# Kernel optimization log

Measured on AMD Instinct MI355X. Metric: run time of the kernel, lower is better.

Reference implementation:

```python
import jax, jax.numpy as jnp
import numpy as np

N = 50000   # nodes
E = 400000  # edges
D = 256     # embedding_dimension
R = 2       # num_relations
NE = 2      # num experts
OUT = 256   # output_size
NEG_SLOPE = 0.01  # nn.LeakyReLU default


def setup_inputs() -> dict:
    key = jax.random.key(0)
    ks = jax.random.split(key, 18)
    s = 0.05
    inp = {
        "des": jax.random.normal(ks[0], (N, 128), jnp.float32),
        "tweet": jax.random.normal(ks[1], (N, 64), jnp.float32),
        "num_prop": jax.random.normal(ks[2], (N, 32), jnp.float32),
        "cat_prop": jax.random.normal(ks[3], (N, 32), jnp.float32),
        "edge_index": jax.random.randint(ks[4], (2, E), 0, N, jnp.int64),
        "edge_type": jax.random.randint(ks[5], (E,), 0, R, jnp.int64),
        # linear_relu_input
        "W_in": jax.random.normal(ks[6], (D, D), jnp.float32) * s,
        "b_in": jnp.zeros((D,), jnp.float32),
        # RGCNConv (shared across the two calls)
        "W_rel": jax.random.normal(ks[7], (R, D, D), jnp.float32) * s,
        "W_root": jax.random.normal(ks[8], (D, D), jnp.float32) * s,
        "b_rgcn": jnp.zeros((D,), jnp.float32),
        # MoE gate + experts (MLP: D -> D -> OUT)
        "w_gate": jax.random.normal(ks[9], (D, NE), jnp.float32) * s,
        "We1": jax.random.normal(ks[10], (NE, D, D), jnp.float32) * s,
        "be1": jnp.zeros((NE, D), jnp.float32),
        "We2": jax.random.normal(ks[11], (NE, D, OUT), jnp.float32) * s,
        "be2": jnp.zeros((NE, OUT), jnp.float32),
    }
    return inp


def _rgcn(x, W_rel, W_root, b, src, dst, edge_type):
    # per-relation node transform, then gather per edge; mean-aggregate per (node, relation)
    h = jnp.einsum('nd,rdh->rnh', x, W_rel)          # (R, N, D)
    msg = h[edge_type, src]                           # (E, D)
    seg = dst * R + edge_type                         # combined (node, relation) segment id
    sums = jax.ops.segment_sum(msg, seg, num_segments=N * R)
    cnt = jax.ops.segment_sum(jnp.ones((E,), msg.dtype), seg, num_segments=N * R)
    agg = sums / jnp.maximum(cnt, 1.0)[:, None]       # per-relation mean (0 if no edges)
    agg = agg.reshape(N, R, -1).sum(axis=1)           # sum over relations
    return x @ W_root + b + agg


def _moe(x, w_gate, We1, be1, We2, be2, k=1):
    # clean (eval) top-k gating: softmax over the top-k logits, scattered into zeros
    logits = x @ w_gate                               # (N, NE)
    top_vals, top_idx = jax.lax.top_k(logits, k)
    gate_vals = jax.nn.softmax(top_vals, axis=-1)     # k=1 -> weight 1.0
    gates = jnp.zeros_like(logits).at[jnp.arange(x.shape[0])[:, None], top_idx].set(gate_vals)
    # compute all experts densely (zero gates annihilate unselected experts)
    h1 = jnp.einsum('nd,edh->enh', x, We1) + be1[:, None, :]
    h1 = jnp.where(h1 >= 0, h1, NEG_SLOPE * h1)       # LeakyReLU
    ye = jnp.einsum('enh,eho->eno', h1, We2) + be2[:, None, :]
    return jnp.einsum('ne,eno->no', gates, ye)


def reference(des, tweet, num_prop, cat_prop, edge_index, edge_type,
              W_in, b_in, W_rel, W_root, b_rgcn, w_gate, We1, be1, We2, be2):
    src, dst = edge_index[0], edge_index[1]
    x = jnp.concatenate((des, tweet, num_prop, cat_prop), axis=1)  # (N, D)
    x = jax.nn.selu(x @ W_in + b_in)
    x = _rgcn(x, W_rel, W_root, b_rgcn, src, dst, edge_type)
    # dropout is identity in eval mode
    x = _rgcn(x, W_rel, W_root, b_rgcn, src, dst, edge_type)
    y = _moe(x, w_gate, We1, be1, We2, be2, k=1)
    return y
```

## Files before the change

kernel.cpp:

```cpp
#include <hip/hip_runtime.h>
#include <cstddef>

static constexpr int N_NODES = 50000;
static constexpr int N_EDGES = 400000;
static constexpr int D = 256;
static constexpr int R = 2;
static constexpr int M_PAD = 50048;
static constexpr int CAP = 32;
static constexpr int NSEG = N_NODES * R;

typedef _Float16 f16x8 __attribute__((ext_vector_type(8)));
typedef short bf16x8 __attribute__((ext_vector_type(8)));
typedef float f32x4 __attribute__((ext_vector_type(4)));

__device__ __forceinline__ unsigned short f2h(float f) {
    _Float16 h = (_Float16)f;
    return *(unsigned short*)&h;
}
__device__ __forceinline__ float h2f(unsigned short u) {
    _Float16 h = *(_Float16*)&u;
    return (float)h;
}
__device__ __forceinline__ unsigned short f2bf(float f) {
    unsigned u = __float_as_uint(f);
    u += 0x7FFF + ((u >> 16) & 1);
    return (unsigned short)(u >> 16);
}
__device__ __forceinline__ float bf2f(unsigned short h) {
    return __uint_as_float((unsigned)h << 16);
}

#define GLOAD16(g, l)                                                          \
    __builtin_amdgcn_global_load_lds(                                          \
        (const __attribute__((address_space(1))) void*)(g),                    \
        (__attribute__((address_space(3))) void*)(l), 16, 0, 0)

struct SSlab { const float* x; int xstr; int kstart; int mload; };
struct SArgs {
    SSlab sl[4];
    int nslab;
    const unsigned short* wt;
    int Ktot;
    int M;
    const float* bias;
    void* out;
};

template<int ACT>
__global__ __launch_bounds__(256, 2)
void sgemm(SArgs a) {
    __shared__ unsigned short As[3][128 * 32];
    __shared__ unsigned short Bs[3][128 * 32];
    const int tid  = threadIdx.x;
    const int wave = tid >> 6, lane = tid & 63;
    const int wm = wave >> 1, wn = wave & 1;
    const int row0 = blockIdx.x * 128;
    const int n0   = blockIdx.y * 128;

    const int arow  = tid >> 1;
    const int ahalf = tid & 1;
    const int br_   = tid >> 2;
    const int bg_   = tid & 3;

    const int gk   = lane >> 4;
    const int frow = lane & 15;
    const int fslot = (gk ^ ((frow >> 1) & 3)) << 3;

    f32x4 acc[4][4] = {};

    for (int ks = 0; ks < a.Ktot; ks += 32) {
        int s = a.nslab - 1;
        while (s > 0 && ks < a.sl[s].kstart) --s;
        const float* xb = a.sl[s].x;
        const int xstr  = a.sl[s].xstr;
        const int kloc  = ks - a.sl[s].kstart;
        const int mload = a.sl[s].mload;

        float ev[16];
        {
            const int gr = row0 + arow;
            if (gr < mload) {
                const float* ap = xb + (size_t)gr * xstr + kloc + ahalf * 16;
                *(float4*)&ev[0]  = ((const float4*)ap)[0];
                *(float4*)&ev[4]  = ((const float4*)ap)[1];
                *(float4*)&ev[8]  = ((const float4*)ap)[2];
                *(float4*)&ev[12] = ((const float4*)ap)[3];
            } else {
                #pragma unroll
                for (int j = 0; j < 16; ++j) ev[j] = 0.f;
            }
        }

        __syncthreads();

        #pragma unroll
        for (int p = 0; p < 3; ++p) {
            #pragma unroll
            for (int q = 0; q < 2; ++q) {
                const int r = q * 64 + br_;
                const int gsrc = (bg_ ^ ((r >> 1) & 3)) << 3;
                GLOAD16(a.wt + (size_t)p * 256 * a.Ktot + (size_t)(n0 + r) * a.Ktot + ks + gsrc,
                        &Bs[p][(q * 64 + wave * 16) * 32]);
            }
        }

        {
            const int sswz = (arow >> 1) & 3;
            #pragma unroll
            for (int g = 0; g < 2; ++g) {
                union { bf16x8 v; unsigned short u[8]; } p1, p2, p3;
                #pragma unroll
                for (int j = 0; j < 8; ++j) {
                    const float v = ev[g * 8 + j];
                    const unsigned short h1 = f2bf(v);
                    const float r1 = v - bf2f(h1);
                    const unsigned short h2 = f2bf(r1);
                    const float r2 = r1 - bf2f(h2);
                    p1.u[j] = h1; p2.u[j] = h2; p3.u[j] = f2bf(r2);
                }
                const int slot = ((ahalf * 2 + g) ^ sswz) << 3;
                *(bf16x8*)&As[0][arow * 32 + slot] = p1.v;
                *(bf16x8*)&As[1][arow * 32 + slot] = p2.v;
                *(bf16x8*)&As[2][arow * 32 + slot] = p3.v;
            }
        }

        __syncthreads();

        bf16x8 bq[4][3];
        #pragma unroll
        for (int n = 0; n < 4; ++n) {
            const int rr = wn * 64 + n * 16 + frow;
            #pragma unroll
            for (int p = 0; p < 3; ++p)
                bq[n][p] = *(const bf16x8*)&Bs[p][rr * 32 + fslot];
        }
        #pragma unroll
        for (int m = 0; m < 4; ++m) {
            const int rr = wm * 64 + m * 16 + frow;
            const bf16x8 a1 = *(const bf16x8*)&As[0][rr * 32 + fslot];
            const bf16x8 a2 = *(const bf16x8*)&As[1][rr * 32 + fslot];
            const bf16x8 a3 = *(const bf16x8*)&As[2][rr * 32 + fslot];
            #pragma unroll
            for (int n = 0; n < 4; ++n) {
                acc[m][n] = __builtin_amdgcn_mfma_f32_16x16x32_bf16(a1, bq[n][0], acc[m][n], 0, 0, 0);
                acc[m][n] = __builtin_amdgcn_mfma_f32_16x16x32_bf16(a1, bq[n][1], acc[m][n], 0, 0, 0);
                acc[m][n] = __builtin_amdgcn_mfma_f32_16x16x32_bf16(a2, bq[n][0], acc[m][n], 0, 0, 0);
                acc[m][n] = __builtin_amdgcn_mfma_f32_16x16x32_bf16(a1, bq[n][2], acc[m][n], 0, 0, 0);
                acc[m][n] = __builtin_amdgcn_mfma_f32_16x16x32_bf16(a3, bq[n][0], acc[m][n], 0, 0, 0);
                acc[m][n] = __builtin_amdgcn_mfma_f32_16x16x32_bf16(a2, bq[n][1], acc[m][n], 0, 0, 0);
            }
        }
    }

    const int erow = (lane >> 4) * 4;
    const int ecol = lane & 15;
    #pragma unroll
    for (int m = 0; m < 4; ++m) {
        #pragma unroll
        for (int r = 0; r < 4; ++r) {
            const int grow = row0 + wm * 64 + m * 16 + erow + r;
            if (grow >= a.M) continue;
            #pragma unroll
            for (int n = 0; n < 4; ++n) {
                const int gcol = n0 + wn * 64 + n * 16 + ecol;
                float v = acc[m][n][r] + a.bias[gcol];
                if (ACT == 1) {
                    const float scale = 1.0507009873554804934f;
                    const float alpha = 1.6732632423543772848f;
                    v = (v > 0.f) ? scale * v : scale * alpha * (expf(v) - 1.f);
                }
                ((float*)a.out)[(size_t)grow * 256 + gcol] = v;
            }
        }
    }
}

struct HSlab { const void* x; int xstr; int kstart; };
struct HArgs {
    HSlab sl[3];
    int nslab;
    const unsigned short* wt;
    int Ktot, M;
    const float* bias;
    const int* sel;
    void* out;
    int ldc;
};

template<int ACT, bool MASK, bool SELB, bool OUTF16, bool A32, bool EZ>
__global__ __launch_bounds__(256, 2)
void hgemm(HArgs a) {
    __shared__ unsigned short As[128 * 64];
    __shared__ unsigned short Bs[128 * 64];
    const int tid  = threadIdx.x;
    const int wave = tid >> 6, lane = tid & 63;
    const int wm = wave >> 1, wn = wave & 1;
    const int row0 = blockIdx.x * 128;
    const int n0   = blockIdx.y * 128;
    const int ex   = EZ ? (int)blockIdx.z : 0;
    const unsigned short* wt = a.wt + (size_t)ex * 65536;
    const float* bias = a.bias + ex * 256;

    const int srow = lane >> 3;
    const int scol = ((lane & 7) ^ (lane >> 3)) << 3;
    const int arow  = tid >> 1;
    const int ahalf = tid & 1;

    f32x4 acc[4][4] = {};

    for (int k0 = 0; k0 < a.Ktot; k0 += 64) {
        int s = a.nslab - 1;
        while (s > 0 && k0 < a.sl[s].kstart) --s;
        const int kloc = k0 - a.sl[s].kstart;
        const int xstr = a.sl[s].xstr;

        float ev[32];
        if (A32) {
            const float* xp = (const float*)a.sl[s].x;
            const float* ap = xp + (size_t)(row0 + arow) * xstr + kloc + ahalf * 32;
            #pragma unroll
            for (int q = 0; q < 8; ++q)
                *(float4*)&ev[q * 4] = ((const float4*)ap)[q];
        }

        __syncthreads();

        if (!A32) {
            const unsigned short* xp = (const unsigned short*)a.sl[s].x;
            #pragma unroll
            for (int i = 0; i < 4; ++i) {
                const int r = wave * 32 + i * 8;
                GLOAD16(xp + (size_t)(row0 + r + srow) * xstr + kloc + scol, &As[r * 64]);
            }
        }
        #pragma unroll
        for (int i = 0; i < 4; ++i) {
            const int r = wave * 32 + i * 8;
            GLOAD16(wt + (size_t)(n0 + r + srow) * a.Ktot + k0 + scol, &Bs[r * 64]);
        }
        if (A32) {
            #pragma unroll
            for (int gi = 0; gi < 4; ++gi) {
                const int sgr = ahalf * 4 + gi;
                union { f16x8 v; _Float16 h[8]; } pk;
                #pragma unroll
                for (int j = 0; j < 8; ++j) pk.h[j] = (_Float16)ev[gi * 8 + j];
                *(f16x8*)&As[arow * 64 + ((sgr ^ (arow & 7)) << 3)] = pk.v;
            }
        }

        __syncthreads();

        #pragma unroll
        for (int kk = 0; kk < 2; ++kk) {
            const int gkk = kk * 4 + (lane >> 4);
            f16x8 af[4], bfr[4];
            #pragma unroll
            for (int m = 0; m < 4; ++m) {
                const int rr = wm * 64 + m * 16 + (lane & 15);
                af[m] = *(const f16x8*)&As[rr * 64 + ((gkk ^ (rr & 7)) << 3)];
            }
            #pragma unroll
            for (int n = 0; n < 4; ++n) {
                const int rr = wn * 64 + n * 16 + (lane & 15);
                bfr[n] = *(const f16x8*)&Bs[rr * 64 + ((gkk ^ (rr & 7)) << 3)];
            }
            #pragma unroll
            for (int m = 0; m < 4; ++m)
                #pragma unroll
                for (int n = 0; n < 4; ++n)
                    acc[m][n] = __builtin_amdgcn_mfma_f32_16x16x32_f16(
                        af[m], bfr[n], acc[m][n], 0, 0, 0);
        }
    }

    const int erow = (lane >> 4) * 4;
    const int ecol = lane & 15;
    #pragma unroll
    for (int m = 0; m < 4; ++m) {
        #pragma unroll
        for (int r = 0; r < 4; ++r) {
            const int grow = row0 + wm * 64 + m * 16 + erow + r;
            if (grow >= a.M) continue;
            int sv = 0;
            if (MASK || SELB) sv = a.sel[grow];
            #pragma unroll
            for (int n = 0; n < 4; ++n) {
                const int gcol = n0 + wn * 64 + n * 16 + ecol;
                const float b = SELB ? a.bias[sv * 256 + gcol] : bias[gcol];
                float v = acc[m][n][r] + b;
                if (ACT == 2) v = (v >= 0.f) ? v : 0.01f * v;
                if (MASK && sv != ex) v = 0.f;
                const size_t oidx = (size_t)grow * a.ldc + (EZ ? ex * 256 : 0) + gcol;
                if (OUTF16) ((unsigned short*)a.out)[oidx] = f2h(v);
                else        ((float*)a.out)[oidx] = v;
            }
        }
    }
}

__global__ __launch_bounds__(256)
void csr_build(const int* __restrict__ ei, const int* __restrict__ et,
               int* cnt, int* slots) {
    const int e = blockIdx.x * 256 + threadIdx.x;
    if (e >= N_EDGES) return;
    const int src = ei[e];
    const int dst = ei[N_EDGES + e];
    const int seg = dst * R + et[e];
    const int slot = atomicAdd(&cnt[seg], 1);
    if (slot < CAP) slots[(size_t)seg * CAP + slot] = src;
}

__global__ __launch_bounds__(256)
void aggregate(const float* __restrict__ X, const int* __restrict__ cnt,
               const int* __restrict__ slots, float* __restrict__ Ab,
               int seg0, int nseg) {
    const int w = blockIdx.x * 4 + (threadIdx.x >> 6);
    if (w >= nseg) return;
    const int lane = threadIdx.x & 63;
    const int s = seg0 + w;
    const int m = min(cnt[s], CAP);
    const int* sl = slots + (size_t)s * CAP;
    float4 acc = make_float4(0.f, 0.f, 0.f, 0.f);
    for (int i = 0; i < m; ++i) {
        const float4 v = *(const float4*)(X + (size_t)sl[i] * 256 + lane * 4);
        acc.x += v.x; acc.y += v.y; acc.z += v.z; acc.w += v.w;
    }
    const float inv = (m > 0) ? 1.0f / (float)m : 0.0f;
    acc.x *= inv; acc.y *= inv; acc.z *= inv; acc.w *= inv;
    *(float4*)(Ab + (size_t)(w >> 1) * 512 + (w & 1) * 256 + lane * 4) = acc;
}

__global__ __launch_bounds__(256)
void agg_h(const unsigned short* __restrict__ Xh, const int* __restrict__ cnt,
           const int* __restrict__ slots, unsigned short* __restrict__ Abh) {
    const int w = blockIdx.x * 4 + (threadIdx.x >> 6);
    if (w >= NSEG) return;
    const int lane = threadIdx.x & 63;
    const int m = min(cnt[w], CAP);
    const int* sl = slots + (size_t)w * CAP;
    float ac[4] = {};
    for (int i = 0; i < m; ++i) {
        const ushort4 v = *(const ushort4*)(Xh + (size_t)sl[i] * 256 + lane * 4);
        ac[0] += h2f(v.x); ac[1] += h2f(v.y); ac[2] += h2f(v.z); ac[3] += h2f(v.w);
    }
    const float inv = (m > 0) ? 1.0f / (float)m : 0.0f;
    ushort4 o = make_ushort4(f2h(ac[0] * inv), f2h(ac[1] * inv),
                             f2h(ac[2] * inv), f2h(ac[3] * inv));
    *(ushort4*)(Abh + (size_t)(w >> 1) * 512 + (w & 1) * 256 + lane * 4) = o;
}

__global__ __launch_bounds__(256)
void fold1(const float* __restrict__ W_root, const float* __restrict__ W_rel,
           const float* __restrict__ b_rg, const float* __restrict__ wg,
           float* __restrict__ wfold, float* __restrict__ c3) {
    const int idx = blockIdx.x * 256 + threadIdx.x;
    if (idx < 1536) {
        const int d = idx / 6, jj = idx % 6, c = jj >> 1, j = jj & 1;
        const float* row = (c == 0) ? W_root + (size_t)d * 256
                                    : W_rel + (size_t)(c - 1) * 65536 + (size_t)d * 256;
        float s = 0.f;
        for (int e = 0; e < 256; ++e) s += row[e] * wg[e * 2 + j];
        wfold[idx] = s;
    } else if (idx < 1538) {
        const int j = idx - 1536;
        float s = 0.f;
        for (int e = 0; e < 256; ++e) s += b_rg[e] * wg[e * 2 + j];
        c3[j] = s;
    }
}

__global__ __launch_bounds__(256)
void fold2(const float* __restrict__ W_root, const float* __restrict__ W_rel,
           const float* __restrict__ b_rg, const float* __restrict__ wfold,
           float* __restrict__ W6, float* __restrict__ cb) {
    const int idx = blockIdx.x * 256 + threadIdx.x;
    if (idx < 4608) {
        const int k = idx / 6, j = idx % 6;
        const float* row = (k < 256) ? W_root + (size_t)k * 256
                                     : W_rel + (size_t)(k - 256) * 256;
        float s = 0.f;
        for (int d = 0; d < 256; ++d) s += row[d] * wfold[d * 6 + j];
        W6[idx] = s;
    } else if (idx < 4614) {
        const int j = idx - 4608;
        float s = 0.f;
        for (int d = 0; d < 256; ++d) s += b_rg[d] * wfold[d * 6 + j];
        cb[j] = s;
    }
}

__global__ __launch_bounds__(256)
void vu_kernel(const float* __restrict__ X1, const float* __restrict__ Ab,
               const float* __restrict__ W6, float* __restrict__ VU, int M) {
    __shared__ float wl[768 * 6];
    for (int i = threadIdx.x; i < 768 * 6; i += 256) wl[i] = W6[i];
    __syncthreads();
    const int wave = threadIdx.x >> 6, lane = threadIdx.x & 63;
    const int n = blockIdx.x * 4 + wave;
    if (n >= M) return;
    const float4 xv = ((const float4*)(X1 + (size_t)n * 256))[lane];
    const float4 a0 = ((const float4*)(Ab + (size_t)n * 512))[lane];
    const float4 a1 = ((const float4*)(Ab + (size_t)n * 512))[lane + 64];
    const float xa[12] = {xv.x, xv.y, xv.z, xv.w, a0.x, a0.y, a0.z, a0.w,
                          a1.x, a1.y, a1.z, a1.w};
    float z[6] = {};
    #pragma unroll
    for (int t = 0; t < 3; ++t)
        #pragma unroll
        for (int i = 0; i < 4; ++i) {
            const int k = t * 256 + lane * 4 + i;
            #pragma unroll
            for (int j = 0; j < 6; ++j) z[j] = fmaf(xa[t * 4 + i], wl[k * 6 + j], z[j]);
        }
    #pragma unroll
    for (int off = 32; off; off >>= 1)
        #pragma unroll
        for (int j = 0; j < 6; ++j) z[j] += __shfl_down(z[j], off, 64);
    if (lane == 0) {
        #pragma unroll
        for (int j = 0; j < 6; ++j) VU[(size_t)n * 6 + j] = z[j];
    }
}

__global__ __launch_bounds__(256)
void u_gate(const float* __restrict__ VU, const int* __restrict__ cnt,
            const int* __restrict__ slots, const float* __restrict__ cb,
            const float* __restrict__ c3, int* __restrict__ sel, int M) {
    const int n = blockIdx.x * 256 + threadIdx.x;
    if (n >= M) return;
    float z0 = VU[(size_t)n * 6 + 0] + cb[0] + c3[0];
    float z1 = VU[(size_t)n * 6 + 1] + cb[1] + c3[1];
    #pragma unroll
    for (int r = 0; r < 2; ++r) {
        const int seg = n * 2 + r;
        const int m = min(cnt[seg], CAP);
        if (m > 0) {
            const int* sl = slots + (size_t)seg * CAP;
            float s0 = 0.f, s1 = 0.f;
            for (int i = 0; i < m; ++i) {
                const int src = sl[i];
                s0 += VU[(size_t)src * 6 + 2 + 2 * r];
                s1 += VU[(size_t)src * 6 + 3 + 2 * r];
            }
            const float inv = 1.0f / (float)m;
            z0 += s0 * inv + cb[2 + 2 * r];
            z1 += s1 * inv + cb[3 + 2 * r];
        }
    }
    sel[n] = (z1 > z0) ? 1 : 0;
}

struct WJ3 { const float* src[4]; unsigned short* dst[4]; int ktot[4]; int koff[4]; };
__global__ __launch_bounds__(256)
void wconv3(WJ3 j) {
    const int job = blockIdx.y;
    const int i = blockIdx.x * 256 + threadIdx.x;
    const int k = i >> 8, n = i & 255;
    const float v = j.src[job][i];
    const unsigned short h1 = f2bf(v);
    const float r1 = v - bf2f(h1);
    const unsigned short h2 = f2bf(r1);
    const float r2 = r1 - bf2f(h2);
    const unsigned short h3 = f2bf(r2);
    const int Kt = j.ktot[job];
    const size_t ps = (size_t)256 * Kt;
    unsigned short* d = j.dst[job] + (size_t)n * Kt + j.koff[job] + k;
    d[0] = h1; d[ps] = h2; d[2 * ps] = h3;
}

struct WJH { const float* src[8]; unsigned short* dst[8]; int stride[8]; int koff[8]; };
__global__ __launch_bounds__(256)
void wconv_h(WJH j) {
    const int job = blockIdx.y;
    const int i = blockIdx.x * 256 + threadIdx.x;
    const int k = i >> 8, n = i & 255;
    j.dst[job][(size_t)n * j.stride[job] + j.koff[job] + k] = f2h(j.src[job][i]);
}

extern "C" void kernel_launch(void* const* d_in, const int* in_sizes, int n_in,
                              void* d_out, int out_size, void* d_ws, size_t ws_size,
                              hipStream_t stream) {
    const float* des    = (const float*)d_in[0];
    const float* twt    = (const float*)d_in[1];
    const float* nump   = (const float*)d_in[2];
    const float* catp   = (const float*)d_in[3];
    const int*   ei     = (const int*)d_in[4];
    const int*   et     = (const int*)d_in[5];
    const float* W_in   = (const float*)d_in[6];
    const float* b_in   = (const float*)d_in[7];
    const float* W_rel  = (const float*)d_in[8];
    const float* W_root = (const float*)d_in[9];
    const float* b_rg   = (const float*)d_in[10];
    const float* w_gate = (const float*)d_in[11];
    const float* We1    = (const float*)d_in[12];
    const float* be1    = (const float*)d_in[13];
    const float* We2    = (const float*)d_in[14];
    const float* be2    = (const float*)d_in[15];

    char* ws = (char*)d_ws;
    size_t off = 0;
    auto alloc = [&](size_t bytes) { char* p = ws + off; off += (bytes + 255) & ~(size_t)255; return p; };
    float* X1f  = (float*)alloc((size_t)M_PAD * 256 * 4);
    char*  regA = alloc((size_t)M_PAD * 512 * 4);
    unsigned short* X2h = (unsigned short*)alloc((size_t)M_PAD * 256 * 2);
    float* VU   = (float*)alloc((size_t)N_NODES * 6 * 4);
    int*   cnt  = (int*)alloc((size_t)NSEG * 4);
    int*   sel  = (int*)alloc((size_t)N_NODES * 4);
    int*   slots= (int*)alloc((size_t)NSEG * CAP * 4);
    unsigned short* wt_in3 = (unsigned short*)alloc((size_t)3 * 65536 * 2);
    unsigned short* wt_rg  = (unsigned short*)alloc((size_t)256 * 768 * 2);
    unsigned short* wt_e1  = (unsigned short*)alloc((size_t)2 * 65536 * 2);
    unsigned short* wt_e2  = (unsigned short*)alloc((size_t)256 * 512 * 2);
    float* wfold = (float*)alloc(256 * 6 * 4);
    float* c3    = (float*)alloc(8);
    float* W6    = (float*)alloc(768 * 6 * 4);
    float* cb    = (float*)alloc(24);

    float* Ab1f = (float*)regA;
    unsigned short* Ab2h = (unsigned short*)regA;
    unsigned short* H    = (unsigned short*)(regA + (size_t)M_PAD * 256 * 4);
    unsigned short* X3h  = (unsigned short*)X1f;

    const dim3 blk(256);

    hipMemsetAsync(cnt, 0, (size_t)NSEG * 4, stream);
    csr_build<<<(N_EDGES + 255) / 256, blk, 0, stream>>>(ei, et, cnt, slots);
    {
        WJ3 j{};
        j.src[0] = W_in; j.dst[0] = wt_in3; j.ktot[0] = 256; j.koff[0] = 0;
        wconv3<<<dim3(256, 1), blk, 0, stream>>>(j);
    }
    {
        WJH j{};
        j.src[0] = W_root;         j.dst[0] = wt_rg;         j.stride[0] = 768; j.koff[0] = 0;
        j.src[1] = W_rel;          j.dst[1] = wt_rg;         j.stride[1] = 768; j.koff[1] = 256;
        j.src[2] = W_rel + 65536;  j.dst[2] = wt_rg;         j.stride[2] = 768; j.koff[2] = 512;
        j.src[3] = We1;            j.dst[3] = wt_e1;         j.stride[3] = 256; j.koff[3] = 0;
        j.src[4] = We1 + 65536;    j.dst[4] = wt_e1 + 65536; j.stride[4] = 256; j.koff[4] = 0;
        j.src[5] = We2;            j.dst[5] = wt_e2;         j.stride[5] = 512; j.koff[5] = 0;
        j.src[6] = We2 + 65536;    j.dst[6] = wt_e2;         j.stride[6] = 512; j.koff[6] = 256;
        wconv_h<<<dim3(256, 7), blk, 0, stream>>>(j);
    }
    fold1<<<7, blk, 0, stream>>>(W_root, W_rel, b_rg, w_gate, wfold, c3);
    fold2<<<19, blk, 0, stream>>>(W_root, W_rel, b_rg, wfold, W6, cb);

    {
        SArgs g{};
        g.sl[0] = {des,  128, 0,   N_NODES};
        g.sl[1] = {twt,  64,  128, N_NODES};
        g.sl[2] = {nump, 32,  192, N_NODES};
        g.sl[3] = {catp, 32,  224, N_NODES};
        g.nslab = 4; g.wt = wt_in3; g.Ktot = 256; g.M = N_NODES;
        g.bias = b_in; g.out = X1f;
        hipLaunchKernelGGL((sgemm<1>), dim3(391, 2), blk, 0, stream, g);
    }

    aggregate<<<(NSEG + 3) / 4, blk, 0, stream>>>(X1f, cnt, slots, Ab1f, 0, NSEG);

    vu_kernel<<<(N_NODES + 3) / 4, blk, 0, stream>>>(X1f, Ab1f, W6, VU, N_NODES);
    u_gate<<<(N_NODES + 255) / 256, blk, 0, stream>>>(VU, cnt, slots, cb, c3, sel, N_NODES);

    {
        HArgs g{};
        g.sl[0] = {X1f,        256, 0};
        g.sl[1] = {Ab1f,       512, 256};
        g.sl[2] = {Ab1f + 256, 512, 512};
        g.nslab = 3; g.wt = wt_rg; g.Ktot = 768; g.M = N_NODES;
        g.bias = b_rg; g.out = X2h; g.ldc = 256;
        hipLaunchKernelGGL((hgemm<0, false, false, true, true, false>),
                           dim3(391, 2), blk, 0, stream, g);
    }

    agg_h<<<(NSEG + 3) / 4, blk, 0, stream>>>(X2h, cnt, slots, Ab2h);

    {
        HArgs g{};
        g.sl[0] = {X2h,        256, 0};
        g.sl[1] = {Ab2h,       512, 256};
        g.sl[2] = {Ab2h + 256, 512, 512};
        g.nslab = 3; g.wt = wt_rg; g.Ktot = 768; g.M = N_NODES;
        g.bias = b_rg; g.out = X3h; g.ldc = 256;
        hipLaunchKernelGGL((hgemm<0, false, false, true, false, false>),
                           dim3(391, 2), blk, 0, stream, g);
    }

    {
        HArgs g{};
        g.sl[0] = {X3h, 256, 0};
        g.nslab = 1; g.wt = wt_e1; g.Ktot = 256; g.M = N_NODES;
        g.bias = be1; g.sel = sel; g.out = H; g.ldc = 512;
        hipLaunchKernelGGL((hgemm<2, true, false, true, false, true>),
                           dim3(391, 2, 2), blk, 0, stream, g);
    }

    {
        HArgs g{};
        g.sl[0] = {H, 512, 0};
        g.nslab = 1; g.wt = wt_e2; g.Ktot = 512; g.M = N_NODES;
        g.bias = be2; g.sel = sel; g.out = d_out; g.ldc = 256;
        hipLaunchKernelGGL((hgemm<0, false, true, false, false, false>),
                           dim3(391, 2), blk, 0, stream, g);
    }
}
```

Before: 492.6 us.

## Route MoE experts via permutation and use two-term fp16 split in input GEMM

Result: faster. 476.6 us (-3.3%).

```diff
diff --git a/kernel.cpp b/kernel.cpp
--- a/kernel.cpp
+++ b/kernel.cpp
@@ -10,7 +10,6 @@
 static constexpr int NSEG = N_NODES * R;
 
 typedef _Float16 f16x8 __attribute__((ext_vector_type(8)));
-typedef short bf16x8 __attribute__((ext_vector_type(8)));
 typedef float f32x4 __attribute__((ext_vector_type(4)));
 
 __device__ __forceinline__ unsigned short f2h(float f) {
@@ -20,14 +19,6 @@
 __device__ __forceinline__ float h2f(unsigned short u) {
     _Float16 h = *(_Float16*)&u;
     return (float)h;
-}
-__device__ __forceinline__ unsigned short f2bf(float f) {
-    unsigned u = __float_as_uint(f);
-    u += 0x7FFF + ((u >> 16) & 1);
-    return (unsigned short)(u >> 16);
-}
-__device__ __forceinline__ float bf2f(unsigned short h) {
-    return __uint_as_float((unsigned)h << 16);
 }
 
 #define GLOAD16(g, l)                                                          \
@@ -49,8 +40,8 @@
 template<int ACT>
 __global__ __launch_bounds__(256, 2)
 void sgemm(SArgs a) {
-    __shared__ unsigned short As[3][128 * 32];
-    __shared__ unsigned short Bs[3][128 * 32];
+    __shared__ unsigned short As[2][128 * 32];
+    __shared__ unsigned short Bs[2][128 * 32];
     const int tid  = threadIdx.x;
     const int wave = tid >> 6, lane = tid & 63;
     const int wm = wave >> 1, wn = wave & 1;
@@ -66,7 +57,8 @@
     const int frow = lane & 15;
     const int fslot = (gk ^ ((frow >> 1) & 3)) << 3;
 
-    f32x4 acc[4][4] = {};
+    f32x4 acc0[4][4] = {};
+    f32x4 accC[4][4] = {};
 
     for (int ks = 0; ks < a.Ktot; ks += 32) {
         int s = a.nslab - 1;
@@ -94,7 +86,7 @@
         __syncthreads();
 
         #pragma unroll
-        for (int p = 0; p < 3; ++p) {
+        for (int p = 0; p < 2; ++p) {
             #pragma unroll
             for (int q = 0; q < 2; ++q) {
                 const int r = q * 64 + br_;
@@ -108,47 +100,40 @@
             const int sswz = (arow >> 1) & 3;
             #pragma unroll
             for (int g = 0; g < 2; ++g) {
-                union { bf16x8 v; unsigned short u[8]; } p1, p2, p3;
+                union { f16x8 v; _Float16 h[8]; } p1, p2;
                 #pragma unroll
                 for (int j = 0; j < 8; ++j) {
                     const float v = ev[g * 8 + j];
-                    const unsigned short h1 = f2bf(v);
-                    const float r1 = v - bf2f(h1);
-                    const unsigned short h2 = f2bf(r1);
-                    const float r2 = r1 - bf2f(h2);
-                    p1.u[j] = h1; p2.u[j] = h2; p3.u[j] = f2bf(r2);
+                    const _Float16 h1 = (_Float16)v;
+                    const float r1 = (v - (float)h1) * 2048.0f;
+                    p1.h[j] = h1; p2.h[j] = (_Float16)r1;
                 }
                 const int slot = ((ahalf * 2 + g) ^ sswz) << 3;
-                *(bf16x8*)&As[0][arow * 32 + slot] = p1.v;
-                *(bf16x8*)&As[1][arow * 32 + slot] = p2.v;
-                *(bf16x8*)&As[2][arow * 32 + slot] = p3.v;
+                *(f16x8*)&As[0][arow * 32 + slot] = p1.v;
+                *(f16x8*)&As[1][arow * 32 + slot] = p2.v;
             }
         }
 
         __syncthreads();
 
-        bf16x8 bq[4][3];
+        f16x8 bq[4][2];
         #pragma unroll
         for (int n = 0; n < 4; ++n) {
             const int rr = wn * 64 + n * 16 + frow;
             #pragma unroll
-            for (int p = 0; p < 3; ++p)
-                bq[n][p] = *(const bf16x8*)&Bs[p][rr * 32 + fslot];
+            for (int p = 0; p < 2; ++p)
+                bq[n][p] = *(const f16x8*)&Bs[p][rr * 32 + fslot];
         }
         #pragma unroll
         for (int m = 0; m < 4; ++m) {
             const int rr = wm * 64 + m * 16 + frow;
-            const bf16x8 a1 = *(const bf16x8*)&As[0][rr * 32 + fslot];
-            const bf16x8 a2 = *(const bf16x8*)&As[1][rr * 32 + fslot];
-            const bf16x8 a3 = *(const bf16x8*)&As[2][rr * 32 + fslot];
+            const f16x8 a1 = *(const f16x8*)&As[0][rr * 32 + fslot];
+            const f16x8 a2 = *(const f16x8*)&As[1][rr * 32 + fslot];
             #pragma unroll
             for (int n = 0; n < 4; ++n) {
-                acc[m][n] = __builtin_amdgcn_mfma_f32_16x16x32_bf16(a1, bq[n][0], acc[m][n], 0, 0, 0);
-                acc[m][n] = __builtin_amdgcn_mfma_f32_16x16x32_bf16(a1, bq[n][1], acc[m][n], 0, 0, 0);
-                acc[m][n] = __builtin_amdgcn_mfma_f32_16x16x32_bf16(a2, bq[n][0], acc[m][n], 0, 0, 0);
-                acc[m][n] = __builtin_amdgcn_mfma_f32_16x16x32_bf16(a1, bq[n][2], acc[m][n], 0, 0, 0);
-                acc[m][n] = __builtin_amdgcn_mfma_f32_16x16x32_bf16(a3, bq[n][0], acc[m][n], 0, 0, 0);
-                acc[m][n] = __builtin_amdgcn_mfma_f32_16x16x32_bf16(a2, bq[n][1], acc[m][n], 0, 0, 0);
+                acc0[m][n] = __builtin_amdgcn_mfma_f32_16x16x32_f16(a1, bq[n][0], acc0[m][n], 0, 0, 0);
+                accC[m][n] = __builtin_amdgcn_mfma_f32_16x16x32_f16(a1, bq[n][1], accC[m][n], 0, 0, 0);
+                accC[m][n] = __builtin_amdgcn_mfma_f32_16x16x32_f16(a2, bq[n][0], accC[m][n], 0, 0, 0);
             }
         }
     }
@@ -164,7 +149,7 @@
             #pragma unroll
             for (int n = 0; n < 4; ++n) {
                 const int gcol = n0 + wn * 64 + n * 16 + ecol;
-                float v = acc[m][n][r] + a.bias[gcol];
+                float v = acc0[m][n][r] + accC[m][n][r] * (1.0f / 2048.0f) + a.bias[gcol];
                 if (ACT == 1) {
                     const float scale = 1.0507009873554804934f;
                     const float alpha = 1.6732632423543772848f;
@@ -184,11 +169,13 @@
     int Ktot, M;
     const float* bias;
     const int* sel;
+    const int* perm;
+    const int* c01;
     void* out;
     int ldc;
 };
 
-template<int ACT, bool MASK, bool SELB, bool OUTF16, bool A32, bool EZ>
+template<int ACT, bool MASK, bool SELB, bool OUTF16, bool A32, bool EZ, bool PERM>
 __global__ __launch_bounds__(256, 2)
 void hgemm(HArgs a) {
     __shared__ unsigned short As[128 * 64];
@@ -202,6 +189,14 @@
     const unsigned short* wt = a.wt + (size_t)ex * 65536;
     const float* bias = a.bias + ex * 256;
 
+    int cntE = 0, base = 0;
+    if (PERM) {
+        const int c0 = a.c01[0];
+        cntE = (ex == 0) ? c0 : a.M - c0;
+        base = (ex == 0) ? 0 : c0;
+        if (row0 >= cntE) return;
+    }
+
     const int srow = lane >> 3;
     const int scol = ((lane & 7) ^ (lane >> 3)) << 3;
     const int arow  = tid >> 1;
@@ -231,7 +226,9 @@
             #pragma unroll
             for (int i = 0; i < 4; ++i) {
                 const int r = wave * 32 + i * 8;
-                GLOAD16(xp + (size_t)(row0 + r + srow) * xstr + kloc + scol, &As[r * 64]);
+                int lr = row0 + r + srow;
+                if (PERM) lr = a.perm[base + (lr < cntE ? lr : cntE - 1)];
+                GLOAD16(xp + (size_t)lr * xstr + kloc + scol, &As[r * 64]);
             }
         }
         #pragma unroll
@@ -282,9 +279,11 @@
         #pragma unroll
         for (int r = 0; r < 4; ++r) {
             const int grow = row0 + wm * 64 + m * 16 + erow + r;
-            if (grow >= a.M) continue;
+            if (PERM) { if (grow >= cntE) continue; }
+            else      { if (grow >= a.M) continue; }
+            const int orow = PERM ? a.perm[base + grow] : grow;
             int sv = 0;
-            if (MASK || SELB) sv = a.sel[grow];
+            if (MASK || SELB) sv = a.sel[orow];
             #pragma unroll
             for (int n = 0; n < 4; ++n) {
                 const int gcol = n0 + wn * 64 + n * 16 + ecol;
@@ -292,7 +291,7 @@
                 float v = acc[m][n][r] + b;
                 if (ACT == 2) v = (v >= 0.f) ? v : 0.01f * v;
                 if (MASK && sv != ex) v = 0.f;
-                const size_t oidx = (size_t)grow * a.ldc + (EZ ? ex * 256 : 0) + gcol;
+                const size_t oidx = (size_t)orow * a.ldc + ((EZ && !PERM) ? ex * 256 : 0) + gcol;
                 if (OUTF16) ((unsigned short*)a.out)[oidx] = f2h(v);
                 else        ((float*)a.out)[oidx] = v;
             }
@@ -452,22 +451,23 @@
     sel[n] = (z1 > z0) ? 1 : 0;
 }
 
-struct WJ3 { const float* src[4]; unsigned short* dst[4]; int ktot[4]; int koff[4]; };
-__global__ __launch_bounds__(256)
-void wconv3(WJ3 j) {
-    const int job = blockIdx.y;
+__global__ __launch_bounds__(256)
+void build_perm(const int* __restrict__ sel, int* __restrict__ perm, int* c01) {
+    const int n = blockIdx.x * 256 + threadIdx.x;
+    if (n >= N_NODES) return;
+    if (sel[n] == 0) perm[atomicAdd(&c01[0], 1)] = n;
+    else             perm[N_NODES - 1 - atomicAdd(&c01[1], 1)] = n;
+}
+
+__global__ __launch_bounds__(256)
+void wconv2(const float* __restrict__ src, unsigned short* __restrict__ dst) {
     const int i = blockIdx.x * 256 + threadIdx.x;
     const int k = i >> 8, n = i & 255;
-    const float v = j.src[job][i];
-    const unsigned short h1 = f2bf(v);
-    const float r1 = v - bf2f(h1);
-    const unsigned short h2 = f2bf(r1);
-    const float r2 = r1 - bf2f(h2);
-    const unsigned short h3 = f2bf(r2);
-    const int Kt = j.ktot[job];
-    const size_t ps = (size_t)256 * Kt;
-    unsigned short* d = j.dst[job] + (size_t)n * Kt + j.koff[job] + k;
-    d[0] = h1; d[ps] = h2; d[2 * ps] = h3;
+    const float v = src[i];
+    const _Float16 h1 = (_Float16)v;
+    const float r1 = (v - (float)h1) * 2048.0f;
+    dst[(size_t)n * 256 + k] = f2h(v);
+    dst[65536 + (size_t)n * 256 + k] = *(unsigned short*)&h1 == 0 ? f2h(r1) : f2h(r1);
 }
 
 struct WJH { const float* src[8]; unsigned short* dst[8]; int stride[8]; int koff[8]; };
@@ -508,11 +508,13 @@
     float* VU   = (float*)alloc((size_t)N_NODES * 6 * 4);
     int*   cnt  = (int*)alloc((size_t)NSEG * 4);
     int*   sel  = (int*)alloc((size_t)N_NODES * 4);
+    int*   perm = (int*)alloc((size_t)N_NODES * 4);
+    int*   c01  = (int*)alloc(256);
     int*   slots= (int*)alloc((size_t)NSEG * CAP * 4);
-    unsigned short* wt_in3 = (unsigned short*)alloc((size_t)3 * 65536 * 2);
+    unsigned short* wt_in2 = (unsigned short*)alloc((size_t)2 * 65536 * 2);
     unsigned short* wt_rg  = (unsigned short*)alloc((size_t)256 * 768 * 2);
     unsigned short* wt_e1  = (unsigned short*)alloc((size_t)2 * 65536 * 2);
-    unsigned short* wt_e2  = (unsigned short*)alloc((size_t)256 * 512 * 2);
+    unsigned short* wt_e2  = (unsigned short*)alloc((size_t)2 * 65536 * 2);
     float* wfold = (float*)alloc(256 * 6 * 4);
     float* c3    = (float*)alloc(8);
     float* W6    = (float*)alloc(768 * 6 * 4);
@@ -520,18 +522,15 @@
 
     float* Ab1f = (float*)regA;
     unsigned short* Ab2h = (unsigned short*)regA;
-    unsigned short* H    = (unsigned short*)(regA + (size_t)M_PAD * 256 * 4);
+    unsigned short* H    = (unsigned short*)(regA + (size_t)M_PAD * 512 * 2);
     unsigned short* X3h  = (unsigned short*)X1f;
 
     const dim3 blk(256);
 
     hipMemsetAsync(cnt, 0, (size_t)NSEG * 4, stream);
+    hipMemsetAsync(c01, 0, 8, stream);
     csr_build<<<(N_EDGES + 255) / 256, blk, 0, stream>>>(ei, et, cnt, slots);
-    {
-        WJ3 j{};
-        j.src[0] = W_in; j.dst[0] = wt_in3; j.ktot[0] = 256; j.koff[0] = 0;
-        wconv3<<<dim3(256, 1), blk, 0, stream>>>(j);
-    }
+    wconv2<<<256, blk, 0, stream>>>(W_in, wt_in2);
     {
         WJH j{};
         j.src[0] = W_root;         j.dst[0] = wt_rg;         j.stride[0] = 768; j.koff[0] = 0;
@@ -539,8 +538,8 @@
         j.src[2] = W_rel + 65536;  j.dst[2] = wt_rg;         j.stride[2] = 768; j.koff[2] = 512;
         j.src[3] = We1;            j.dst[3] = wt_e1;         j.stride[3] = 256; j.koff[3] = 0;
         j.src[4] = We1 + 65536;    j.dst[4] = wt_e1 + 65536; j.stride[4] = 256; j.koff[4] = 0;
-        j.src[5] = We2;            j.dst[5] = wt_e2;         j.stride[5] = 512; j.koff[5] = 0;
-        j.src[6] = We2 + 65536;    j.dst[6] = wt_e2;         j.stride[6] = 512; j.koff[6] = 256;
+        j.src[5] = We2;            j.dst[5] = wt_e2;         j.stride[5] = 256; j.koff[5] = 0;
+        j.src[6] = We2 + 65536;    j.dst[6] = wt_e2 + 65536; j.stride[6] = 256; j.koff[6] = 0;
         wconv_h<<<dim3(256, 7), blk, 0, stream>>>(j);
     }
     fold1<<<7, blk, 0, stream>>>(W_root, W_rel, b_rg, w_gate, wfold, c3);
@@ -552,7 +551,7 @@
         g.sl[1] = {twt,  64,  128, N_NODES};
         g.sl[2] = {nump, 32,  192, N_NODES};
         g.sl[3] = {catp, 32,  224, N_NODES};
-        g.nslab = 4; g.wt = wt_in3; g.Ktot = 256; g.M = N_NODES;
+        g.nslab = 4; g.wt = wt_in2; g.Ktot = 256; g.M = N_NODES;
         g.bias = b_in; g.out = X1f;
         hipLaunchKernelGGL((sgemm<1>), dim3(391, 2), blk, 0, stream, g);
     }
@@ -561,6 +560,7 @@
 
     vu_kernel<<<(N_NODES + 3) / 4, blk, 0, stream>>>(X1f, Ab1f, W6, VU, N_NODES);
     u_gate<<<(N_NODES + 255) / 256, blk, 0, stream>>>(VU, cnt, slots, cb, c3, sel, N_NODES);
+    build_perm<<<(N_NODES + 255) / 256, blk, 0, stream>>>(sel, perm, c01);
 
     {
         HArgs g{};
@@ -569,7 +569,7 @@
         g.sl[2] = {Ab1f + 256, 512, 512};
         g.nslab = 3; g.wt = wt_rg; g.Ktot = 768; g.M = N_NODES;
         g.bias = b_rg; g.out = X2h; g.ldc = 256;
-        hipLaunchKernelGGL((hgemm<0, false, false, true, true, false>),
+        hipLaunchKernelGGL((hgemm<0, false, false, true, true, false, false>),
                            dim3(391, 2), blk, 0, stream, g);
     }
 
@@ -582,7 +582,7 @@
         g.sl[2] = {Ab2h + 256, 512, 512};
         g.nslab = 3; g.wt = wt_rg; g.Ktot = 768; g.M = N_NODES;
         g.bias = b_rg; g.out = X3h; g.ldc = 256;
-        hipLaunchKernelGGL((hgemm<0, false, false, true, false, false>),
+        hipLaunchKernelGGL((hgemm<0, false, false, true, false, false, false>),
                            dim3(391, 2), blk, 0, stream, g);
     }
 
@@ -590,17 +590,17 @@
         HArgs g{};
         g.sl[0] = {X3h, 256, 0};
         g.nslab = 1; g.wt = wt_e1; g.Ktot = 256; g.M = N_NODES;
-        g.bias = be1; g.sel = sel; g.out = H; g.ldc = 512;
-        hipLaunchKernelGGL((hgemm<2, true, false, true, false, true>),
+        g.bias = be1; g.perm = perm; g.c01 = c01; g.out = H; g.ldc = 256;
+        hipLaunchKernelGGL((hgemm<2, false, false, true, false, true, true>),
                            dim3(391, 2, 2), blk, 0, stream, g);
     }
 
     {
         HArgs g{};
-        g.sl[0] = {H, 512, 0};
-        g.nslab = 1; g.wt = wt_e2; g.Ktot = 512; g.M = N_NODES;
-        g.bias = be2; g.sel = sel; g.out = d_out; g.ldc = 256;
-        hipLaunchKernelGGL((hgemm<0, false, true, false, false, false>),
-                           dim3(391, 2), blk, 0, stream, g);
-    }
-}
+        g.sl[0] = {H, 256, 0};
+        g.nslab = 1; g.wt = wt_e2; g.Ktot = 256; g.M = N_NODES;
+        g.bias = be2; g.perm = perm; g.c01 = c01; g.out = d_out; g.ldc = 256;
+        hipLaunchKernelGGL((hgemm<0, false, false, false, false, true, true>),
+                           dim3(391, 2, 2), blk, 0, stream, g);
+    }
+}
```
